# Kernel tuning notes

Hardware: AMD Instinct MI355X
Metric: run time of the kernel (lower is better)

## Reference

```python
import jax, jax.numpy as jnp
import numpy as np

FEAT_DIM = 4
TOKEN_DIM = 256
HIDDEN = [256, 256]
B, N, T = 512, 512, 4
BN_EPS = 1e-5


def setup_inputs() -> dict:
    key = jax.random.key(0)
    ks = jax.random.split(key, 10)
    bbox_ltwh = jax.random.uniform(ks[0], (B, N, T, FEAT_DIM), dtype=jnp.float32)
    mask = jax.random.randint(ks[1], (B, N), 0, 2).astype(bool)
    # MLP params: Linear(4->256)+BN+ReLU, Linear(256->256)+BN+ReLU, Linear(256->256)
    def lin(k, fan_in, fan_out):
        bound = 1.0 / np.sqrt(fan_in)
        kw, kb = jax.random.split(k)
        W = jax.random.uniform(kw, (fan_in, fan_out), minval=-bound, maxval=bound, dtype=jnp.float32)
        b = jax.random.uniform(kb, (fan_out,), minval=-bound, maxval=bound, dtype=jnp.float32)
        return W, b
    W1, b1 = lin(ks[2], FEAT_DIM, HIDDEN[0])
    W2, b2 = lin(ks[3], HIDDEN[0], HIDDEN[1])
    W3, b3 = lin(ks[4], HIDDEN[1], TOKEN_DIM)
    g1 = jnp.ones((HIDDEN[0],), jnp.float32); be1 = jnp.zeros((HIDDEN[0],), jnp.float32)
    g2 = jnp.ones((HIDDEN[1],), jnp.float32); be2 = jnp.zeros((HIDDEN[1],), jnp.float32)
    return {"bbox_ltwh": bbox_ltwh, "mask": mask,
            "W1": W1, "b1": b1, "g1": g1, "be1": be1,
            "W2": W2, "b2": b2, "g2": g2, "be2": be2,
            "W3": W3, "b3": b3}


def _masked_bn(h, m, cnt, gamma, beta):
    # BatchNorm1d (training mode) over only the valid (masked-in) rows.
    mu = jnp.sum(h * m, axis=0) / cnt
    var = jnp.sum(jnp.square(h - mu) * m, axis=0) / cnt
    return (h - mu) * jax.lax.rsqrt(var + BN_EPS) * gamma + beta


def reference(bbox_ltwh, mask, W1, b1, g1, be1, W2, b2, g2, be2, W3, b3):
    # last bbox of each tracklet: [B, N, 4] -> [B*N, 4]
    x = bbox_ltwh[:, :, 0].reshape(-1, FEAT_DIM)
    m = mask.reshape(-1).astype(x.dtype)[:, None]  # [B*N, 1]
    cnt = jnp.maximum(jnp.sum(m), 1.0)
    # Equivalent to gather(valid) -> MLP -> scatter into zeros: compute on all
    # rows with BN statistics taken over valid rows only, then zero invalid rows.
    h = jax.nn.relu(_masked_bn(x @ W1 + b1, m, cnt, g1, be1))
    h = jax.nn.relu(_masked_bn(h @ W2 + b2, m, cnt, g2, be2))
    h = h @ W3 + b3
    out = (h * m).reshape(B, N, TOKEN_DIM)
    return out
```

## Files before the change

### kernel.cpp

```cpp
#include <hip/hip_runtime.h>

typedef __attribute__((ext_vector_type(8))) short short8;
typedef __attribute__((ext_vector_type(4))) float f32x4;

#define M_ROWS (512*512)
#define NTILES (M_ROWS/64)
#define GRID_STATS 512
#define GRID_MLP 256
#define TILES_PER_BLK (NTILES/GRID_MLP)
#define BN_EPS_F 1e-5f

#define WS_FLAG 0
#define WS_P1   64
#define WS_CNT  8192
#define WS_A1   8256
#define WS_D1   9280
#define WS_A2   9536
#define WS_C2   9792
#define WS_W2T  10240
#define WS_W3T  43008
#define WS_P2   76800

__device__ __forceinline__ float load_mask(const void* mp, int fmt, int row) {
  return fmt ? (((const unsigned char*)mp)[row] ? 1.f : 0.f)
             : (((const int*)mp)[row] ? 1.f : 0.f);
}

__device__ __forceinline__ ushort f2bf(float f) {
  unsigned int u = __float_as_uint(f);
  u += 0x7FFFu + ((u >> 16) & 1u);
  return (ushort)(u >> 16);
}

__device__ __forceinline__ void barrier_lds() {
  __builtin_amdgcn_sched_barrier(0);
  asm volatile("s_waitcnt lgkmcnt(0)");
  __builtin_amdgcn_sched_barrier(0);
  __builtin_amdgcn_s_barrier();
  __builtin_amdgcn_sched_barrier(0);
}

__global__ void detect_mask_kernel(const unsigned char* __restrict__ mb,
                                   int* __restrict__ flag) {
  __shared__ int any;
  if (threadIdx.x == 0) any = 0;
  __syncthreads();
  int c = 0;
  for (int i = threadIdx.x; i < 4096; i += blockDim.x)
    if ((i & 3) && mb[i]) c = 1;
  if (c) atomicOr(&any, 1);
  __syncthreads();
  if (threadIdx.x == 0) *flag = any;
}

__global__ __launch_bounds__(256) void stats1_kernel(
    const float* __restrict__ bbox, const void* __restrict__ maskp,
    const int* __restrict__ flagp, float* __restrict__ part) {
  const int t = threadIdx.x;
  const int fmt = *flagp;
  float cnt = 0.f, sx[4] = {0.f,0.f,0.f,0.f}, sxx[16];
  #pragma unroll
  for (int i = 0; i < 16; ++i) sxx[i] = 0.f;
  for (int row = blockIdx.x * 256 + t; row < M_ROWS; row += gridDim.x * 256) {
    float m = load_mask(maskp, fmt, row);
    if (m != 0.f) {
      float4 x = *(const float4*)(bbox + (size_t)row * 16);
      float xv[4] = {x.x, x.y, x.z, x.w};
      cnt += 1.f;
      #pragma unroll
      for (int i = 0; i < 4; ++i) {
        sx[i] += xv[i];
        #pragma unroll
        for (int j = 0; j < 4; ++j) sxx[i*4+j] = fmaf(xv[i], xv[j], sxx[i*4+j]);
      }
    }
  }
  __shared__ float rb[256][22];
  rb[t][0] = cnt;
  #pragma unroll
  for (int i = 0; i < 4; ++i) rb[t][1+i] = sx[i];
  #pragma unroll
  for (int i = 0; i < 16; ++i) rb[t][5+i] = sxx[i];
  __syncthreads();
  for (int off = 128; off > 0; off >>= 1) {
    if (t < off) {
      #pragma unroll
      for (int s = 0; s < 21; ++s) rb[t][s] += rb[t+off][s];
    }
    __syncthreads();
  }
  if (t < 21) part[blockIdx.x * 24 + t] = rb[0][t];
}

__global__ __launch_bounds__(256) void finalize1_kernel(
    const float* __restrict__ part, const float* __restrict__ W1,
    const float* __restrict__ b1, const float* __restrict__ g1,
    const float* __restrict__ be1, float* __restrict__ wsf) {
  const int t = threadIdx.x;
  __shared__ float s[21];
  if (t < 21) {
    float a = 0.f;
    for (int b = 0; b < 256; ++b) a += part[b*24 + t];
    s[t] = a;
  }
  __syncthreads();
  const float cnt = fmaxf(s[0], 1.f);
  float w[4] = {W1[t], W1[256+t], W1[512+t], W1[768+t]};
  const float b1f = b1[t];
  float sw = 0.f;
  #pragma unroll
  for (int k = 0; k < 4; ++k) sw = fmaf(s[1+k], w[k], sw);
  float qf = 0.f;
  #pragma unroll
  for (int i = 0; i < 4; ++i)
    #pragma unroll
    for (int j = 0; j < 4; ++j) qf = fmaf(s[5+i*4+j]*w[i], w[j], qf);
  const float mu  = sw/cnt + b1f;
  const float eh2 = (qf + 2.f*b1f*sw)/cnt + b1f*b1f;
  const float var = fmaxf(eh2 - mu*mu, 0.f);
  const float a1  = g1[t] * rsqrtf(var + BN_EPS_F);
  const float c1  = be1[t] - mu*a1;
  #pragma unroll
  for (int k = 0; k < 4; ++k) wsf[WS_A1 + k*256 + t] = w[k]*a1;
  wsf[WS_D1 + t] = fmaf(b1f, a1, c1);
  if (t == 0) wsf[WS_CNT] = cnt;
}

__global__ __launch_bounds__(256) void prep_weights(
    const float* __restrict__ W2, const float* __restrict__ W3,
    float* __restrict__ wsf) {
  const int n = blockIdx.x & 255;
  const int t = threadIdx.x;
  const float* W = (blockIdx.x < 256) ? W2 : W3;
  ushort* dst = (ushort*)(wsf + ((blockIdx.x < 256) ? WS_W2T : WS_W3T));
  dst[n*256 + t] = f2bf(W[t*256 + n]);
}

__device__ __forceinline__ void compute_h1(
    const float (*xs)[4], ushort* h1s, int t,
    const float a1c[4][2], const float d1c[2]) {
  const int c0 = (t & 127) * 2;
  const int r0 = (t >> 7) * 32;
  #pragma unroll 4
  for (int rr = 0; rr < 32; ++rr) {
    const int r = r0 + rr;
    const f32x4 xv = *(const f32x4*)&xs[r][0];
    float v0 = d1c[0], v1 = d1c[1];
    v0 = fmaf(xv.x, a1c[0][0], v0); v1 = fmaf(xv.x, a1c[0][1], v1);
    v0 = fmaf(xv.y, a1c[1][0], v0); v1 = fmaf(xv.y, a1c[1][1], v1);
    v0 = fmaf(xv.z, a1c[2][0], v0); v1 = fmaf(xv.z, a1c[2][1], v1);
    v0 = fmaf(xv.w, a1c[3][0], v0); v1 = fmaf(xv.w, a1c[3][1], v1);
    v0 = fmaxf(v0, 0.f); v1 = fmaxf(v1, 0.f);
    unsigned int pk = (unsigned int)f2bf(v0) | ((unsigned int)f2bf(v1) << 16);
    unsigned int byte = (unsigned int)r*512u + (unsigned int)c0*2u;
    byte ^= (unsigned int)(r & 7) << 4;
    *(unsigned int*)((char*)h1s + byte) = pk;
  }
}

__device__ __forceinline__ void load_aF(const ushort* h1s, int lane, int ks,
                                        int kb, short8 aF[4]) {
  #pragma unroll
  for (int rf = 0; rf < 4; ++rf) {
    const int row = rf*16 + (lane & 15);
    unsigned int byte = (unsigned int)row*512u + (unsigned int)((ks*32 + kb)*2);
    byte ^= (unsigned int)(row & 7) << 4;
    aF[rf] = *(const short8*)((const char*)h1s + byte);
  }
}

__device__ __forceinline__ void gemm_reg(const ushort* h1s,
    const short8 Br[4][8], int lane, f32x4 acc[4][4]) {
  const int kb = (lane >> 4) * 8;
  #pragma unroll
  for (int ks = 0; ks < 8; ++ks) {
    short8 aF[4];
    load_aF(h1s, lane, ks, kb, aF);
    #pragma unroll
    for (int cf = 0; cf < 4; ++cf)
      #pragma unroll
      for (int rf = 0; rf < 4; ++rf)
        acc[rf][cf] = __builtin_amdgcn_mfma_f32_16x16x32_bf16(
            aF[rf], Br[cf][ks], acc[rf][cf], 0, 0, 0);
  }
}

__device__ __forceinline__ void load_B(const ushort* __restrict__ Wt,
                                       int lane, int wave, short8 Br[4][8]) {
  const int kb = (lane >> 4) * 8;
  const ushort* wp = Wt + (size_t)(wave*64 + (lane & 15))*256 + kb;
  #pragma unroll
  for (int cf = 0; cf < 4; ++cf)
    #pragma unroll
    for (int ks = 0; ks < 8; ++ks)
      Br[cf][ks] = *(const short8*)(wp + cf*4096 + ks*32);
}

__global__ __launch_bounds__(256, 2) void stats2_mfma(
    const float* __restrict__ bbox, const void* __restrict__ maskp,
    const int* __restrict__ flagp, const float* wsf,
    const float* __restrict__ b2, float* __restrict__ part2) {
  __shared__ float xs[64][4];
  __shared__ float ms[64];
  __shared__ ushort h1s[64*256];
  const int t = threadIdx.x, lane = t & 63, wave = t >> 6;
  const int fmt = *flagp;
  float a1c[4][2], d1c[2];
  {
    const int c0 = (t & 127) * 2;
    #pragma unroll
    for (int j = 0; j < 4; ++j) {
      a1c[j][0] = wsf[WS_A1 + j*256 + c0];
      a1c[j][1] = wsf[WS_A1 + j*256 + c0 + 1];
    }
    d1c[0] = wsf[WS_D1 + c0]; d1c[1] = wsf[WS_D1 + c0 + 1];
  }
  short8 B2r[4][8];
  load_B((const ushort*)(wsf + WS_W2T), lane, wave, B2r);
  float b2v[4];
  #pragma unroll
  for (int cf = 0; cf < 4; ++cf) b2v[cf] = b2[wave*64 + cf*16 + (lane & 15)];
  float pS[4] = {0,0,0,0}, pQ[4] = {0,0,0,0};

  for (int tile = blockIdx.x; tile < NTILES; tile += GRID_STATS) {
    const int row0 = tile << 6;
    __syncthreads();
    if (t < 64) {
      float4 x4 = *(const float4*)(bbox + (size_t)(row0 + t) * 16);
      xs[t][0] = x4.x; xs[t][1] = x4.y; xs[t][2] = x4.z; xs[t][3] = x4.w;
      ms[t] = load_mask(maskp, fmt, row0 + t);
    }
    __syncthreads();
    compute_h1(xs, h1s, t, a1c, d1c);
    __syncthreads();
    f32x4 acc[4][4];
    #pragma unroll
    for (int rf = 0; rf < 4; ++rf)
      #pragma unroll
      for (int cf = 0; cf < 4; ++cf)
        acc[rf][cf] = (f32x4){b2v[cf], b2v[cf], b2v[cf], b2v[cf]};
    gemm_reg(h1s, B2r, lane, acc);
    float mr[4][4];
    #pragma unroll
    for (int rf = 0; rf < 4; ++rf)
      #pragma unroll
      for (int r = 0; r < 4; ++r)
        mr[rf][r] = ms[rf*16 + ((lane >> 4) * 4) + r];
    #pragma unroll
    for (int cf = 0; cf < 4; ++cf)
      #pragma unroll
      for (int rf = 0; rf < 4; ++rf)
        #pragma unroll
        for (int r = 0; r < 4; ++r) {
          const float m = mr[rf][r];
          const float v = acc[rf][cf][r];
          pS[cf] = fmaf(m, v, pS[cf]);
          pQ[cf] = fmaf(m*v, v, pQ[cf]);
        }
  }
  #pragma unroll
  for (int cf = 0; cf < 4; ++cf) {
    pS[cf] += __shfl_xor(pS[cf], 16); pS[cf] += __shfl_xor(pS[cf], 32);
    pQ[cf] += __shfl_xor(pQ[cf], 16); pQ[cf] += __shfl_xor(pQ[cf], 32);
  }
  if (lane < 16) {
    #pragma unroll
    for (int cf = 0; cf < 4; ++cf) {
      const int col = wave*64 + cf*16 + lane;
      part2[(size_t)blockIdx.x*512 + col] = pS[cf];
      part2[(size_t)blockIdx.x*512 + 256 + col] = pQ[cf];
    }
  }
}

__global__ __launch_bounds__(256) void finalize2_kernel(
    float* __restrict__ wsf, const float* __restrict__ g2,
    const float* __restrict__ be2) {
  const int f = blockIdx.x, t = threadIdx.x;
  const float* part2 = wsf + WS_P2;
  float s1 = 0.f, s2 = 0.f;
  for (int b = t; b < GRID_STATS; b += 256) {
    s1 += part2[(size_t)b*512 + f];
    s2 += part2[(size_t)b*512 + 256 + f];
  }
  __shared__ float r1[256], r2[256];
  r1[t] = s1; r2[t] = s2;
  __syncthreads();
  for (int off = 128; off > 0; off >>= 1) {
    if (t < off) { r1[t] += r1[t+off]; r2[t] += r2[t+off]; }
    __syncthreads();
  }
  if (t == 0) {
    const float cnt = wsf[WS_CNT];
    const float mu  = r1[0]/cnt;
    const float var = fmaxf(r2[0]/cnt - mu*mu, 0.f);
    const float a2  = g2[f] * rsqrtf(var + BN_EPS_F);
    wsf[WS_A2 + f] = a2;
    wsf[WS_C2 + f] = be2[f] - mu*a2;
  }
}

__global__ __launch_bounds__(256, 1) void mlp3_mfma(
    const float* __restrict__ bbox, const void* __restrict__ maskp,
    const int* __restrict__ flagp, const float* wsf,
    const float* __restrict__ b2, const float* __restrict__ b3,
    float* __restrict__ out) {
  __shared__ ushort h1s[64*256];
  __shared__ float xst[TILES_PER_BLK*64][4];
  __shared__ float mst[TILES_PER_BLK*64];
  const int t = threadIdx.x, lane = t & 63, wave = t >> 6;
  const int fmt = *flagp;
  const int row_base = blockIdx.x * (TILES_PER_BLK*64);

  #pragma unroll
  for (int i = 0; i < TILES_PER_BLK*64/256; ++i) {
    const int r = i*256 + t;
    float4 x4 = *(const float4*)(bbox + (size_t)(row_base + r) * 16);
    xst[r][0] = x4.x; xst[r][1] = x4.y; xst[r][2] = x4.z; xst[r][3] = x4.w;
    mst[r] = load_mask(maskp, fmt, row_base + r);
  }
  float a1c[4][2], d1c[2];
  {
    const int c0 = (t & 127) * 2;
    #pragma unroll
    for (int j = 0; j < 4; ++j) {
      a1c[j][0] = wsf[WS_A1 + j*256 + c0];
      a1c[j][1] = wsf[WS_A1 + j*256 + c0 + 1];
    }
    d1c[0] = wsf[WS_D1 + c0]; d1c[1] = wsf[WS_D1 + c0 + 1];
  }
  short8 B2r[4][8], B3r[4][8];
  load_B((const ushort*)(wsf + WS_W2T), lane, wave, B2r);
  load_B((const ushort*)(wsf + WS_W3T), lane, wave, B3r);
  float b2v[4], b3v[4], a2v[4], c2v[4];
  #pragma unroll
  for (int cf = 0; cf < 4; ++cf) {
    const int col = wave*64 + cf*16 + (lane & 15);
    b2v[cf] = b2[col]; b3v[cf] = b3[col];
    a2v[cf] = wsf[WS_A2 + col]; c2v[cf] = wsf[WS_C2 + col];
  }
  __syncthreads();

  for (int tile = 0; tile < TILES_PER_BLK; ++tile) {
    const int r0 = tile * 64;
    compute_h1(&xst[r0], h1s, t, a1c, d1c);
    barrier_lds();
    f32x4 acc[4][4];
    #pragma unroll
    for (int rf = 0; rf < 4; ++rf)
      #pragma unroll
      for (int cf = 0; cf < 4; ++cf)
        acc[rf][cf] = (f32x4){b2v[cf], b2v[cf], b2v[cf], b2v[cf]};
    gemm_reg(h1s, B2r, lane, acc);
    barrier_lds();
    #pragma unroll
    for (int rf = 0; rf < 4; ++rf)
      #pragma unroll
      for (int cf = 0; cf < 4; ++cf) {
        const int col = wave*64 + cf*16 + (lane & 15);
        #pragma unroll
        for (int r = 0; r < 4; ++r) {
          const float v = fmaxf(fmaf(acc[rf][cf][r], a2v[cf], c2v[cf]), 0.f);
          const int row = rf*16 + ((lane >> 4) * 4) + r;
          unsigned int byte = (unsigned int)row*512u + (unsigned int)col*2u;
          byte ^= (unsigned int)(row & 7) << 4;
          *(ushort*)((char*)h1s + byte) = f2bf(v);
        }
      }
    barrier_lds();
    #pragma unroll
    for (int rf = 0; rf < 4; ++rf)
      #pragma unroll
      for (int cf = 0; cf < 4; ++cf)
        acc[rf][cf] = (f32x4){b3v[cf], b3v[cf], b3v[cf], b3v[cf]};
    gemm_reg(h1s, B3r, lane, acc);
    float mr[4][4];
    #pragma unroll
    for (int rf = 0; rf < 4; ++rf)
      #pragma unroll
      for (int r = 0; r < 4; ++r)
        mr[rf][r] = mst[r0 + rf*16 + ((lane >> 4) * 4) + r];
    #pragma unroll
    for (int rf = 0; rf < 4; ++rf)
      #pragma unroll
      for (int cf = 0; cf < 4; ++cf) {
        const int col = wave*64 + cf*16 + (lane & 15);
        #pragma unroll
        for (int r = 0; r < 4; ++r) {
          const int lrow = rf*16 + ((lane >> 4) * 4) + r;
          out[(size_t)(row_base + r0 + lrow)*256 + col] =
              acc[rf][cf][r] * mr[rf][r];
        }
      }
    barrier_lds();
  }
}

extern "C" void kernel_launch(void* const* d_in, const int* in_sizes, int n_in,
                              void* d_out, int out_size, void* d_ws, size_t ws_size,
                              hipStream_t stream) {
  (void)in_sizes; (void)n_in; (void)out_size; (void)ws_size;
  const float* bbox = (const float*)d_in[0];
  const void*  maskp= d_in[1];
  const float* W1 = (const float*)d_in[2];
  const float* b1 = (const float*)d_in[3];
  const float* g1 = (const float*)d_in[4];
  const float* be1= (const float*)d_in[5];
  const float* W2 = (const float*)d_in[6];
  const float* b2 = (const float*)d_in[7];
  const float* g2 = (const float*)d_in[8];
  const float* be2= (const float*)d_in[9];
  const float* W3 = (const float*)d_in[10];
  const float* b3 = (const float*)d_in[11];
  float* out = (float*)d_out;
  float* wsf = (float*)d_ws;
  int*   flag= (int*)d_ws;

  hipLaunchKernelGGL(detect_mask_kernel, dim3(1), dim3(256), 0, stream,
                     (const unsigned char*)maskp, flag);
  hipLaunchKernelGGL(stats1_kernel, dim3(256), dim3(256), 0, stream,
                     bbox, maskp, flag, wsf + WS_P1);
  hipLaunchKernelGGL(finalize1_kernel, dim3(1), dim3(256), 0, stream,
                     wsf + WS_P1, W1, b1, g1, be1, wsf);
  hipLaunchKernelGGL(prep_weights, dim3(512), dim3(256), 0, stream,
                     W2, W3, wsf);
  hipLaunchKernelGGL(stats2_mfma, dim3(GRID_STATS), dim3(256), 0, stream,
                     bbox, maskp, flag, wsf, b2, wsf + WS_P2);
  hipLaunchKernelGGL(finalize2_kernel, dim3(256), dim3(256), 0, stream,
                     wsf, g2, be2);
  hipLaunchKernelGGL(mlp3_mfma, dim3(GRID_MLP), dim3(256), 0, stream,
                     bbox, maskp, flag, wsf, b2, b3, out);
}
```

Baseline: 217.1 us.

## Fuse all MLP stages into one cooperative kernel with grid syncs

Replaces the seven-kernel pipeline with a single cooperative kernel of 256 blocks. It computes layer-1 stats, weight transpose, layer-2 stats and the final MLP, separated by grid-wide syncs. Each block keeps its 1024 input rows and masks resident in LDS across phases, so bbox is read once instead of three times. Launch overhead is also reduced. In exchange it runs only 256 blocks with one block per CU, adds three grid barriers, and the weight transpose now writes in a strided pattern. The old multi-kernel path remains as a fallback if the cooperative launch fails.

```diff
diff --git a/kernel.cpp b/kernel.cpp
--- a/kernel.cpp
+++ b/kernel.cpp
@@ -1,16 +1,21 @@
 #include <hip/hip_runtime.h>
+#include <hip/hip_cooperative_groups.h>
+
+namespace cg = cooperative_groups;
 
 typedef __attribute__((ext_vector_type(8))) short short8;
 typedef __attribute__((ext_vector_type(4))) float f32x4;
 
 #define M_ROWS (512*512)
 #define NTILES (M_ROWS/64)
+#define GRID_N 256
+#define ROWS_PER_BLK (M_ROWS/GRID_N)
+#define TILES_PER_BLK (ROWS_PER_BLK/64)
 #define GRID_STATS 512
 #define GRID_MLP 256
-#define TILES_PER_BLK (NTILES/GRID_MLP)
+#define TPB_FALL (NTILES/GRID_MLP)
 #define BN_EPS_F 1e-5f
 
-#define WS_FLAG 0
 #define WS_P1   64
 #define WS_CNT  8192
 #define WS_A1   8256
@@ -38,102 +43,6 @@
   __builtin_amdgcn_sched_barrier(0);
   __builtin_amdgcn_s_barrier();
   __builtin_amdgcn_sched_barrier(0);
-}
-
-__global__ void detect_mask_kernel(const unsigned char* __restrict__ mb,
-                                   int* __restrict__ flag) {
-  __shared__ int any;
-  if (threadIdx.x == 0) any = 0;
-  __syncthreads();
-  int c = 0;
-  for (int i = threadIdx.x; i < 4096; i += blockDim.x)
-    if ((i & 3) && mb[i]) c = 1;
-  if (c) atomicOr(&any, 1);
-  __syncthreads();
-  if (threadIdx.x == 0) *flag = any;
-}
-
-__global__ __launch_bounds__(256) void stats1_kernel(
-    const float* __restrict__ bbox, const void* __restrict__ maskp,
-    const int* __restrict__ flagp, float* __restrict__ part) {
-  const int t = threadIdx.x;
-  const int fmt = *flagp;
-  float cnt = 0.f, sx[4] = {0.f,0.f,0.f,0.f}, sxx[16];
-  #pragma unroll
-  for (int i = 0; i < 16; ++i) sxx[i] = 0.f;
-  for (int row = blockIdx.x * 256 + t; row < M_ROWS; row += gridDim.x * 256) {
-    float m = load_mask(maskp, fmt, row);
-    if (m != 0.f) {
-      float4 x = *(const float4*)(bbox + (size_t)row * 16);
-      float xv[4] = {x.x, x.y, x.z, x.w};
-      cnt += 1.f;
-      #pragma unroll
-      for (int i = 0; i < 4; ++i) {
-        sx[i] += xv[i];
-        #pragma unroll
-        for (int j = 0; j < 4; ++j) sxx[i*4+j] = fmaf(xv[i], xv[j], sxx[i*4+j]);
-      }
-    }
-  }
-  __shared__ float rb[256][22];
-  rb[t][0] = cnt;
-  #pragma unroll
-  for (int i = 0; i < 4; ++i) rb[t][1+i] = sx[i];
-  #pragma unroll
-  for (int i = 0; i < 16; ++i) rb[t][5+i] = sxx[i];
-  __syncthreads();
-  for (int off = 128; off > 0; off >>= 1) {
-    if (t < off) {
-      #pragma unroll
-      for (int s = 0; s < 21; ++s) rb[t][s] += rb[t+off][s];
-    }
-    __syncthreads();
-  }
-  if (t < 21) part[blockIdx.x * 24 + t] = rb[0][t];
-}
-
-__global__ __launch_bounds__(256) void finalize1_kernel(
-    const float* __restrict__ part, const float* __restrict__ W1,
-    const float* __restrict__ b1, const float* __restrict__ g1,
-    const float* __restrict__ be1, float* __restrict__ wsf) {
-  const int t = threadIdx.x;
-  __shared__ float s[21];
-  if (t < 21) {
-    float a = 0.f;
-    for (int b = 0; b < 256; ++b) a += part[b*24 + t];
-    s[t] = a;
-  }
-  __syncthreads();
-  const float cnt = fmaxf(s[0], 1.f);
-  float w[4] = {W1[t], W1[256+t], W1[512+t], W1[768+t]};
-  const float b1f = b1[t];
-  float sw = 0.f;
-  #pragma unroll
-  for (int k = 0; k < 4; ++k) sw = fmaf(s[1+k], w[k], sw);
-  float qf = 0.f;
-  #pragma unroll
-  for (int i = 0; i < 4; ++i)
-    #pragma unroll
-    for (int j = 0; j < 4; ++j) qf = fmaf(s[5+i*4+j]*w[i], w[j], qf);
-  const float mu  = sw/cnt + b1f;
-  const float eh2 = (qf + 2.f*b1f*sw)/cnt + b1f*b1f;
-  const float var = fmaxf(eh2 - mu*mu, 0.f);
-  const float a1  = g1[t] * rsqrtf(var + BN_EPS_F);
-  const float c1  = be1[t] - mu*a1;
-  #pragma unroll
-  for (int k = 0; k < 4; ++k) wsf[WS_A1 + k*256 + t] = w[k]*a1;
-  wsf[WS_D1 + t] = fmaf(b1f, a1, c1);
-  if (t == 0) wsf[WS_CNT] = cnt;
-}
-
-__global__ __launch_bounds__(256) void prep_weights(
-    const float* __restrict__ W2, const float* __restrict__ W3,
-    float* __restrict__ wsf) {
-  const int n = blockIdx.x & 255;
-  const int t = threadIdx.x;
-  const float* W = (blockIdx.x < 256) ? W2 : W3;
-  ushort* dst = (ushort*)(wsf + ((blockIdx.x < 256) ? WS_W2T : WS_W3T));
-  dst[n*256 + t] = f2bf(W[t*256 + n]);
 }
 
 __device__ __forceinline__ void compute_h1(
@@ -196,6 +105,362 @@
       Br[cf][ks] = *(const short8*)(wp + cf*4096 + ks*32);
 }
 
+__global__ void __launch_bounds__(256, 1) fused_all(
+    const float* __restrict__ bbox, const void* __restrict__ maskp,
+    const float* __restrict__ W1, const float* __restrict__ b1,
+    const float* __restrict__ g1, const float* __restrict__ be1,
+    const float* __restrict__ W2, const float* __restrict__ b2,
+    const float* __restrict__ g2, const float* __restrict__ be2,
+    const float* __restrict__ W3, const float* __restrict__ b3,
+    float* __restrict__ out, float* __restrict__ wsf) {
+  cg::grid_group grid = cg::this_grid();
+  __shared__ float xst[ROWS_PER_BLK][4];
+  __shared__ float mst[ROWS_PER_BLK];
+  __shared__ ushort h1s[64*256];
+  __shared__ int s_fmt;
+  float (*red)[24] = (float (*)[24])(void*)h1s;
+  const int t = threadIdx.x, lane = t & 63, wave = t >> 6;
+  const int b = blockIdx.x;
+  const int row_base = b * ROWS_PER_BLK;
+
+  if (t == 0) s_fmt = 0;
+  __syncthreads();
+  {
+    const uint4 v = ((const uint4*)maskp)[t];
+    if (((v.x | v.y | v.z | v.w) & 0xFFFFFF00u) != 0u) s_fmt = 1;
+  }
+  __syncthreads();
+  const int fmt = s_fmt;
+
+  {
+    float cnt = 0.f, sx[4] = {0.f,0.f,0.f,0.f}, sxx[16];
+    #pragma unroll
+    for (int i = 0; i < 16; ++i) sxx[i] = 0.f;
+    #pragma unroll
+    for (int i = 0; i < ROWS_PER_BLK/256; ++i) {
+      const int r = i*256 + t;
+      float4 x4 = *(const float4*)(bbox + (size_t)(row_base + r) * 16);
+      xst[r][0] = x4.x; xst[r][1] = x4.y; xst[r][2] = x4.z; xst[r][3] = x4.w;
+      const float m = load_mask(maskp, fmt, row_base + r);
+      mst[r] = m;
+      if (m != 0.f) {
+        float xv[4] = {x4.x, x4.y, x4.z, x4.w};
+        cnt += 1.f;
+        #pragma unroll
+        for (int i2 = 0; i2 < 4; ++i2) {
+          sx[i2] += xv[i2];
+          #pragma unroll
+          for (int j = 0; j < 4; ++j)
+            sxx[i2*4+j] = fmaf(xv[i2], xv[j], sxx[i2*4+j]);
+        }
+      }
+    }
+    red[t][0] = cnt;
+    #pragma unroll
+    for (int i = 0; i < 4; ++i) red[t][1+i] = sx[i];
+    #pragma unroll
+    for (int i = 0; i < 16; ++i) red[t][5+i] = sxx[i];
+    __syncthreads();
+    for (int off = 128; off > 0; off >>= 1) {
+      if (t < off) {
+        #pragma unroll
+        for (int s = 0; s < 21; ++s) red[t][s] += red[t+off][s];
+      }
+      __syncthreads();
+    }
+    if (t < 21) wsf[WS_P1 + b*24 + t] = red[0][t];
+  }
+  {
+    ((ushort*)(wsf + WS_W2T))[t*256 + b] = f2bf(W2[b*256 + t]);
+    ((ushort*)(wsf + WS_W3T))[t*256 + b] = f2bf(W3[b*256 + t]);
+  }
+  grid.sync();
+
+  float a1c[4][2], d1c[2], cnt_all;
+  {
+    #pragma unroll
+    for (int s = 0; s < 21; ++s) red[t][s] = wsf[WS_P1 + t*24 + s];
+    __syncthreads();
+    for (int off = 128; off > 0; off >>= 1) {
+      if (t < off) {
+        #pragma unroll
+        for (int s = 0; s < 21; ++s) red[t][s] += red[t+off][s];
+      }
+      __syncthreads();
+    }
+    float s[21];
+    #pragma unroll
+    for (int i = 0; i < 21; ++i) s[i] = red[0][i];
+    __syncthreads();
+    cnt_all = fmaxf(s[0], 1.f);
+    const int c0 = (t & 127) * 2;
+    #pragma unroll
+    for (int cc = 0; cc < 2; ++cc) {
+      const int f = c0 + cc;
+      float w[4] = {W1[f], W1[256+f], W1[512+f], W1[768+f]};
+      const float b1f = b1[f];
+      float sw = 0.f;
+      #pragma unroll
+      for (int k = 0; k < 4; ++k) sw = fmaf(s[1+k], w[k], sw);
+      float qf = 0.f;
+      #pragma unroll
+      for (int i = 0; i < 4; ++i)
+        #pragma unroll
+        for (int j = 0; j < 4; ++j) qf = fmaf(s[5+i*4+j]*w[i], w[j], qf);
+      const float mu  = sw/cnt_all + b1f;
+      const float eh2 = (qf + 2.f*b1f*sw)/cnt_all + b1f*b1f;
+      const float var = fmaxf(eh2 - mu*mu, 0.f);
+      const float a1  = g1[f] * rsqrtf(var + BN_EPS_F);
+      const float c1  = be1[f] - mu*a1;
+      #pragma unroll
+      for (int k = 0; k < 4; ++k) a1c[k][cc] = w[k]*a1;
+      d1c[cc] = fmaf(b1f, a1, c1);
+    }
+  }
+
+  short8 B2r[4][8];
+  load_B((const ushort*)(wsf + WS_W2T), lane, wave, B2r);
+  float b2v[4];
+  #pragma unroll
+  for (int cf = 0; cf < 4; ++cf) b2v[cf] = b2[wave*64 + cf*16 + (lane & 15)];
+  {
+    float pS[4] = {0,0,0,0}, pQ[4] = {0,0,0,0};
+    for (int tile = 0; tile < TILES_PER_BLK; ++tile) {
+      compute_h1(&xst[tile*64], h1s, t, a1c, d1c);
+      __syncthreads();
+      f32x4 acc[4][4];
+      #pragma unroll
+      for (int rf = 0; rf < 4; ++rf)
+        #pragma unroll
+        for (int cf = 0; cf < 4; ++cf)
+          acc[rf][cf] = (f32x4){b2v[cf], b2v[cf], b2v[cf], b2v[cf]};
+      gemm_reg(h1s, B2r, lane, acc);
+      #pragma unroll
+      for (int rf = 0; rf < 4; ++rf) {
+        #pragma unroll
+        for (int r = 0; r < 4; ++r) {
+          const float m = mst[tile*64 + rf*16 + ((lane >> 4) * 4) + r];
+          #pragma unroll
+          for (int cf = 0; cf < 4; ++cf) {
+            const float v = acc[rf][cf][r];
+            pS[cf] = fmaf(m, v, pS[cf]);
+            pQ[cf] = fmaf(m*v, v, pQ[cf]);
+          }
+        }
+      }
+      __syncthreads();
+    }
+    #pragma unroll
+    for (int cf = 0; cf < 4; ++cf) {
+      pS[cf] += __shfl_xor(pS[cf], 16); pS[cf] += __shfl_xor(pS[cf], 32);
+      pQ[cf] += __shfl_xor(pQ[cf], 16); pQ[cf] += __shfl_xor(pQ[cf], 32);
+    }
+    if (lane < 16) {
+      #pragma unroll
+      for (int cf = 0; cf < 4; ++cf) {
+        const int col = wave*64 + cf*16 + lane;
+        wsf[WS_P2 + (size_t)col*256 + b] = pS[cf];
+        wsf[WS_P2 + (size_t)(256 + col)*256 + b] = pQ[cf];
+      }
+    }
+  }
+  grid.sync();
+
+  {
+    float s1 = wsf[WS_P2 + (size_t)b*256 + t];
+    float s2 = wsf[WS_P2 + (size_t)(256 + b)*256 + t];
+    red[t][0] = s1; red[t][1] = s2;
+    __syncthreads();
+    for (int off = 128; off > 0; off >>= 1) {
+      if (t < off) { red[t][0] += red[t+off][0]; red[t][1] += red[t+off][1]; }
+      __syncthreads();
+    }
+    if (t == 0) {
+      const float mu  = red[0][0]/cnt_all;
+      const float var = fmaxf(red[0][1]/cnt_all - mu*mu, 0.f);
+      const float a2  = g2[b] * rsqrtf(var + BN_EPS_F);
+      wsf[WS_A2 + b] = a2;
+      wsf[WS_C2 + b] = be2[b] - mu*a2;
+    }
+  }
+  grid.sync();
+
+  short8 B3r[4][8];
+  load_B((const ushort*)(wsf + WS_W3T), lane, wave, B3r);
+  float b3v[4], a2v[4], c2v[4];
+  #pragma unroll
+  for (int cf = 0; cf < 4; ++cf) {
+    const int col = wave*64 + cf*16 + (lane & 15);
+    b3v[cf] = b3[col];
+    a2v[cf] = wsf[WS_A2 + col]; c2v[cf] = wsf[WS_C2 + col];
+  }
+  __syncthreads();
+
+  for (int tile = 0; tile < TILES_PER_BLK; ++tile) {
+    const int r0 = tile * 64;
+    compute_h1(&xst[r0], h1s, t, a1c, d1c);
+    barrier_lds();
+    f32x4 acc[4][4];
+    #pragma unroll
+    for (int rf = 0; rf < 4; ++rf)
+      #pragma unroll
+      for (int cf = 0; cf < 4; ++cf)
+        acc[rf][cf] = (f32x4){b2v[cf], b2v[cf], b2v[cf], b2v[cf]};
+    gemm_reg(h1s, B2r, lane, acc);
+    barrier_lds();
+    #pragma unroll
+    for (int rf = 0; rf < 4; ++rf)
+      #pragma unroll
+      for (int cf = 0; cf < 4; ++cf) {
+        const int col = wave*64 + cf*16 + (lane & 15);
+        #pragma unroll
+        for (int r = 0; r < 4; ++r) {
+          const float v = fmaxf(fmaf(acc[rf][cf][r], a2v[cf], c2v[cf]), 0.f);
+          const int row = rf*16 + ((lane >> 4) * 4) + r;
+          unsigned int byte = (unsigned int)row*512u + (unsigned int)col*2u;
+          byte ^= (unsigned int)(row & 7) << 4;
+          *(ushort*)((char*)h1s + byte) = f2bf(v);
+        }
+      }
+    barrier_lds();
+    #pragma unroll
+    for (int rf = 0; rf < 4; ++rf)
+      #pragma unroll
+      for (int cf = 0; cf < 4; ++cf)
+        acc[rf][cf] = (f32x4){b3v[cf], b3v[cf], b3v[cf], b3v[cf]};
+    gemm_reg(h1s, B3r, lane, acc);
+    float mr[4][4];
+    #pragma unroll
+    for (int rf = 0; rf < 4; ++rf)
+      #pragma unroll
+      for (int r = 0; r < 4; ++r)
+        mr[rf][r] = mst[r0 + rf*16 + ((lane >> 4) * 4) + r];
+    #pragma unroll
+    for (int rf = 0; rf < 4; ++rf)
+      #pragma unroll
+      for (int cf = 0; cf < 4; ++cf) {
+        const int col = wave*64 + cf*16 + (lane & 15);
+        #pragma unroll
+        for (int r = 0; r < 4; ++r) {
+          const int lrow = rf*16 + ((lane >> 4) * 4) + r;
+          out[(size_t)(row_base + r0 + lrow)*256 + col] =
+              acc[rf][cf][r] * mr[rf][r];
+        }
+      }
+    barrier_lds();
+  }
+}
+
+__global__ void detect_mask_kernel(const unsigned char* __restrict__ mb,
+                                   int* __restrict__ flag) {
+  __shared__ int any;
+  if (threadIdx.x == 0) any = 0;
+  __syncthreads();
+  int c = 0;
+  for (int i = threadIdx.x; i < 4096; i += blockDim.x)
+    if ((i & 3) && mb[i]) c = 1;
+  if (c) atomicOr(&any, 1);
+  __syncthreads();
+  if (threadIdx.x == 0) *flag = any;
+}
+
+__global__ __launch_bounds__(256) void stats1_kernel(
+    const float* __restrict__ bbox, const void* __restrict__ maskp,
+    const int* __restrict__ flagp, float* __restrict__ part) {
+  const int t = threadIdx.x;
+  const int fmt = *flagp;
+  float cnt = 0.f, sx[4] = {0.f,0.f,0.f,0.f}, sxx[16];
+  #pragma unroll
+  for (int i = 0; i < 16; ++i) sxx[i] = 0.f;
+  for (int row = blockIdx.x * 256 + t; row < M_ROWS; row += gridDim.x * 256) {
+    float m = load_mask(maskp, fmt, row);
+    if (m != 0.f) {
+      float4 x = *(const float4*)(bbox + (size_t)row * 16);
+      float xv[4] = {x.x, x.y, x.z, x.w};
+      cnt += 1.f;
+      #pragma unroll
+      for (int i = 0; i < 4; ++i) {
+        sx[i] += xv[i];
+        #pragma unroll
+        for (int j = 0; j < 4; ++j) sxx[i*4+j] = fmaf(xv[i], xv[j], sxx[i*4+j]);
+      }
+    }
+  }
+  __shared__ float rb[256][22];
+  rb[t][0] = cnt;
+  #pragma unroll
+  for (int i = 0; i < 4; ++i) rb[t][1+i] = sx[i];
+  #pragma unroll
+  for (int i = 0; i < 16; ++i) rb[t][5+i] = sxx[i];
+  __syncthreads();
+  for (int off = 128; off > 0; off >>= 1) {
+    if (t < off) {
+      #pragma unroll
+      for (int s = 0; s < 21; ++s) rb[t][s] += rb[t+off][s];
+    }
+    __syncthreads();
+  }
+  if (t < 21) part[blockIdx.x * 24 + t] = rb[0][t];
+}
+
+__global__ __launch_bounds__(256) void finalize1_kernel(
+    const float* __restrict__ part, const float* __restrict__ W1,
+    const float* __restrict__ b1, const float* __restrict__ g1,
+    const float* __restrict__ be1, float* __restrict__ wsf) {
+  const int t = threadIdx.x;
+  __shared__ float s[21];
+  if (t < 21) {
+    float a = 0.f;
+    for (int b = 0; b < 256; ++b) a += part[b*24 + t];
+    s[t] = a;
+  }
+  __syncthreads();
+  const float cnt = fmaxf(s[0], 1.f);
+  float w[4] = {W1[t], W1[256+t], W1[512+t], W1[768+t]};
+  const float b1f = b1[t];
+  float sw = 0.f;
+  #pragma unroll
+  for (int k = 0; k < 4; ++k) sw = fmaf(s[1+k], w[k], sw);
+  float qf = 0.f;
+  #pragma unroll
+  for (int i = 0; i < 4; ++i)
+    #pragma unroll
+    for (int j = 0; j < 4; ++j) qf = fmaf(s[5+i*4+j]*w[i], w[j], qf);
+  const float mu  = sw/cnt + b1f;
+  const float eh2 = (qf + 2.f*b1f*sw)/cnt + b1f*b1f;
+  const float var = fmaxf(eh2 - mu*mu, 0.f);
+  const float a1  = g1[t] * rsqrtf(var + BN_EPS_F);
+  const float c1  = be1[t] - mu*a1;
+  #pragma unroll
+  for (int k = 0; k < 4; ++k) wsf[WS_A1 + k*256 + t] = w[k]*a1;
+  wsf[WS_D1 + t] = fmaf(b1f, a1, c1);
+  if (t == 0) wsf[WS_CNT] = cnt;
+}
+
+__global__ __launch_bounds__(256) void prep_weights(
+    const float* __restrict__ W2, const float* __restrict__ W3,
+    float* __restrict__ wsf) {
+  const int n = blockIdx.x & 255;
+  const int t = threadIdx.x;
+  const float* W = (blockIdx.x < 256) ? W2 : W3;
+  ushort* dst = (ushort*)(wsf + ((blockIdx.x < 256) ? WS_W2T : WS_W3T));
+  dst[n*256 + t] = f2bf(W[t*256 + n]);
+}
+
+__device__ __forceinline__ void fb_compute_h1(
+    const float (*xs)[4], ushort* h1s, int t,
+    const float* wsf) {
+  float a1c[4][2], d1c[2];
+  const int c0 = (t & 127) * 2;
+  #pragma unroll
+  for (int j = 0; j < 4; ++j) {
+    a1c[j][0] = wsf[WS_A1 + j*256 + c0];
+    a1c[j][1] = wsf[WS_A1 + j*256 + c0 + 1];
+  }
+  d1c[0] = wsf[WS_D1 + c0]; d1c[1] = wsf[WS_D1 + c0 + 1];
+  compute_h1(xs, h1s, t, a1c, d1c);
+}
+
 __global__ __launch_bounds__(256, 2) void stats2_mfma(
     const float* __restrict__ bbox, const void* __restrict__ maskp,
     const int* __restrict__ flagp, const float* wsf,
@@ -306,14 +571,14 @@
     const float* __restrict__ b2, const float* __restrict__ b3,
     float* __restrict__ out) {
   __shared__ ushort h1s[64*256];
-  __shared__ float xst[TILES_PER_BLK*64][4];
-  __shared__ float mst[TILES_PER_BLK*64];
+  __shared__ float xst[TPB_FALL*64][4];
+  __shared__ float mst[TPB_FALL*64];
   const int t = threadIdx.x, lane = t & 63, wave = t >> 6;
   const int fmt = *flagp;
-  const int row_base = blockIdx.x * (TILES_PER_BLK*64);
-
-  #pragma unroll
-  for (int i = 0; i < TILES_PER_BLK*64/256; ++i) {
+  const int row_base = blockIdx.x * (TPB_FALL*64);
+
+  #pragma unroll
+  for (int i = 0; i < TPB_FALL*64/256; ++i) {
     const int r = i*256 + t;
     float4 x4 = *(const float4*)(bbox + (size_t)(row_base + r) * 16);
     xst[r][0] = x4.x; xst[r][1] = x4.y; xst[r][2] = x4.z; xst[r][3] = x4.w;
@@ -341,7 +606,7 @@
   }
   __syncthreads();
 
-  for (int tile = 0; tile < TILES_PER_BLK; ++tile) {
+  for (int tile = 0; tile < TPB_FALL; ++tile) {
     const int r0 = tile * 64;
     compute_h1(&xst[r0], h1s, t, a1c, d1c);
     barrier_lds();
@@ -416,18 +681,28 @@
   float* wsf = (float*)d_ws;
   int*   flag= (int*)d_ws;
 
-  hipLaunchKernelGGL(detect_mask_kernel, dim3(1), dim3(256), 0, stream,
-                     (const unsigned char*)maskp, flag);
-  hipLaunchKernelGGL(stats1_kernel, dim3(256), dim3(256), 0, stream,
-                     bbox, maskp, flag, wsf + WS_P1);
-  hipLaunchKernelGGL(finalize1_kernel, dim3(1), dim3(256), 0, stream,
-                     wsf + WS_P1, W1, b1, g1, be1, wsf);
-  hipLaunchKernelGGL(prep_weights, dim3(512), dim3(256), 0, stream,
-                     W2, W3, wsf);
-  hipLaunchKernelGGL(stats2_mfma, dim3(GRID_STATS), dim3(256), 0, stream,
-                     bbox, maskp, flag, wsf, b2, wsf + WS_P2);
-  hipLaunchKernelGGL(finalize2_kernel, dim3(256), dim3(256), 0, stream,
-                     wsf, g2, be2);
-  hipLaunchKernelGGL(mlp3_mfma, dim3(GRID_MLP), dim3(256), 0, stream,
-                     bbox, maskp, flag, wsf, b2, b3, out);
-}
+  void* args[] = {
+    (void*)&bbox, (void*)&maskp, (void*)&W1, (void*)&b1, (void*)&g1,
+    (void*)&be1, (void*)&W2, (void*)&b2, (void*)&g2, (void*)&be2,
+    (void*)&W3, (void*)&b3, (void*)&out, (void*)&wsf
+  };
+  hipError_t err = hipLaunchCooperativeKernel((const void*)fused_all,
+                                              dim3(GRID_N), dim3(256),
+                                              args, 0, stream);
+  if (err != hipSuccess) {
+    hipLaunchKernelGGL(detect_mask_kernel, dim3(1), dim3(256), 0, stream,
+                       (const unsigned char*)maskp, flag);
+    hipLaunchKernelGGL(stats1_kernel, dim3(256), dim3(256), 0, stream,
+                       bbox, maskp, flag, wsf + WS_P1);
+    hipLaunchKernelGGL(finalize1_kernel, dim3(1), dim3(256), 0, stream,
+                       wsf + WS_P1, W1, b1, g1, be1, wsf);
+    hipLaunchKernelGGL(prep_weights, dim3(512), dim3(256), 0, stream,
+                       W2, W3, wsf);
+    hipLaunchKernelGGL(stats2_mfma, dim3(GRID_STATS), dim3(256), 0, stream,
+                       bbox, maskp, flag, wsf, b2, wsf + WS_P2);
+    hipLaunchKernelGGL(finalize2_kernel, dim3(256), dim3(256), 0, stream,
+                       wsf, g2, be2);
+    hipLaunchKernelGGL(mlp3_mfma, dim3(GRID_MLP), dim3(256), 0, stream,
+                       bbox, maskp, flag, wsf, b2, b3, out);
+  }
+}
```

Measured after the change: 304.2 us. 1.4x slower.

## Merge setup kernels and widen final MLP kernel to 512 threads

Applied to the files above, without the earlier changes.

Folds mask-format detection, first-layer statistics and weight transpose/bf16 conversion into a single setup kernel, removing two launches, and makes each consumer kernel detect the mask format locally instead of reading a flag. The final MLP kernel now uses 512 threads (8 waves), each owning 32 output columns instead of 64. This halves per-wave B registers and accumulators and allows two blocks per CU, aiming for better latency hiding. The cost is a two-stage reduction in finalize1 and extra per-block mask detection work.

```diff
diff --git a/kernel.cpp b/kernel.cpp
--- a/kernel.cpp
+++ b/kernel.cpp
@@ -5,21 +5,22 @@
 
 #define M_ROWS (512*512)
 #define NTILES (M_ROWS/64)
+#define GRID_SETUP 512
 #define GRID_STATS 512
 #define GRID_MLP 256
-#define TILES_PER_BLK (NTILES/GRID_MLP)
+#define ROWS_MLP (M_ROWS/GRID_MLP)
+#define TILES_MLP (ROWS_MLP/64)
 #define BN_EPS_F 1e-5f
 
-#define WS_FLAG 0
 #define WS_P1   64
-#define WS_CNT  8192
-#define WS_A1   8256
-#define WS_D1   9280
-#define WS_A2   9536
-#define WS_C2   9792
-#define WS_W2T  10240
-#define WS_W3T  43008
-#define WS_P2   76800
+#define WS_CNT  12352
+#define WS_A1   12416
+#define WS_D1   13440
+#define WS_A2   13696
+#define WS_C2   13952
+#define WS_W2T  14336
+#define WS_W3T  47104
+#define WS_P2   79872
 
 __device__ __forceinline__ float load_mask(const void* mp, int fmt, int row) {
   return fmt ? (((const unsigned char*)mp)[row] ? 1.f : 0.f)
@@ -38,102 +39,6 @@
   __builtin_amdgcn_sched_barrier(0);
   __builtin_amdgcn_s_barrier();
   __builtin_amdgcn_sched_barrier(0);
-}
-
-__global__ void detect_mask_kernel(const unsigned char* __restrict__ mb,
-                                   int* __restrict__ flag) {
-  __shared__ int any;
-  if (threadIdx.x == 0) any = 0;
-  __syncthreads();
-  int c = 0;
-  for (int i = threadIdx.x; i < 4096; i += blockDim.x)
-    if ((i & 3) && mb[i]) c = 1;
-  if (c) atomicOr(&any, 1);
-  __syncthreads();
-  if (threadIdx.x == 0) *flag = any;
-}
-
-__global__ __launch_bounds__(256) void stats1_kernel(
-    const float* __restrict__ bbox, const void* __restrict__ maskp,
-    const int* __restrict__ flagp, float* __restrict__ part) {
-  const int t = threadIdx.x;
-  const int fmt = *flagp;
-  float cnt = 0.f, sx[4] = {0.f,0.f,0.f,0.f}, sxx[16];
-  #pragma unroll
-  for (int i = 0; i < 16; ++i) sxx[i] = 0.f;
-  for (int row = blockIdx.x * 256 + t; row < M_ROWS; row += gridDim.x * 256) {
-    float m = load_mask(maskp, fmt, row);
-    if (m != 0.f) {
-      float4 x = *(const float4*)(bbox + (size_t)row * 16);
-      float xv[4] = {x.x, x.y, x.z, x.w};
-      cnt += 1.f;
-      #pragma unroll
-      for (int i = 0; i < 4; ++i) {
-        sx[i] += xv[i];
-        #pragma unroll
-        for (int j = 0; j < 4; ++j) sxx[i*4+j] = fmaf(xv[i], xv[j], sxx[i*4+j]);
-      }
-    }
-  }
-  __shared__ float rb[256][22];
-  rb[t][0] = cnt;
-  #pragma unroll
-  for (int i = 0; i < 4; ++i) rb[t][1+i] = sx[i];
-  #pragma unroll
-  for (int i = 0; i < 16; ++i) rb[t][5+i] = sxx[i];
-  __syncthreads();
-  for (int off = 128; off > 0; off >>= 1) {
-    if (t < off) {
-      #pragma unroll
-      for (int s = 0; s < 21; ++s) rb[t][s] += rb[t+off][s];
-    }
-    __syncthreads();
-  }
-  if (t < 21) part[blockIdx.x * 24 + t] = rb[0][t];
-}
-
-__global__ __launch_bounds__(256) void finalize1_kernel(
-    const float* __restrict__ part, const float* __restrict__ W1,
-    const float* __restrict__ b1, const float* __restrict__ g1,
-    const float* __restrict__ be1, float* __restrict__ wsf) {
-  const int t = threadIdx.x;
-  __shared__ float s[21];
-  if (t < 21) {
-    float a = 0.f;
-    for (int b = 0; b < 256; ++b) a += part[b*24 + t];
-    s[t] = a;
-  }
-  __syncthreads();
-  const float cnt = fmaxf(s[0], 1.f);
-  float w[4] = {W1[t], W1[256+t], W1[512+t], W1[768+t]};
-  const float b1f = b1[t];
-  float sw = 0.f;
-  #pragma unroll
-  for (int k = 0; k < 4; ++k) sw = fmaf(s[1+k], w[k], sw);
-  float qf = 0.f;
-  #pragma unroll
-  for (int i = 0; i < 4; ++i)
-    #pragma unroll
-    for (int j = 0; j < 4; ++j) qf = fmaf(s[5+i*4+j]*w[i], w[j], qf);
-  const float mu  = sw/cnt + b1f;
-  const float eh2 = (qf + 2.f*b1f*sw)/cnt + b1f*b1f;
-  const float var = fmaxf(eh2 - mu*mu, 0.f);
-  const float a1  = g1[t] * rsqrtf(var + BN_EPS_F);
-  const float c1  = be1[t] - mu*a1;
-  #pragma unroll
-  for (int k = 0; k < 4; ++k) wsf[WS_A1 + k*256 + t] = w[k]*a1;
-  wsf[WS_D1 + t] = fmaf(b1f, a1, c1);
-  if (t == 0) wsf[WS_CNT] = cnt;
-}
-
-__global__ __launch_bounds__(256) void prep_weights(
-    const float* __restrict__ W2, const float* __restrict__ W3,
-    float* __restrict__ wsf) {
-  const int n = blockIdx.x & 255;
-  const int t = threadIdx.x;
-  const float* W = (blockIdx.x < 256) ? W2 : W3;
-  ushort* dst = (ushort*)(wsf + ((blockIdx.x < 256) ? WS_W2T : WS_W3T));
-  dst[n*256 + t] = f2bf(W[t*256 + n]);
 }
 
 __device__ __forceinline__ void compute_h1(
@@ -158,6 +63,28 @@
   }
 }
 
+__device__ __forceinline__ void compute_h1_512(
+    const float (*xs)[4], ushort* h1s, int t,
+    const float a1c[4][2], const float d1c[2]) {
+  const int c0 = (t & 127) * 2;
+  const int r0 = (t >> 7) * 16;
+  #pragma unroll 4
+  for (int rr = 0; rr < 16; ++rr) {
+    const int r = r0 + rr;
+    const f32x4 xv = *(const f32x4*)&xs[r][0];
+    float v0 = d1c[0], v1 = d1c[1];
+    v0 = fmaf(xv.x, a1c[0][0], v0); v1 = fmaf(xv.x, a1c[0][1], v1);
+    v0 = fmaf(xv.y, a1c[1][0], v0); v1 = fmaf(xv.y, a1c[1][1], v1);
+    v0 = fmaf(xv.z, a1c[2][0], v0); v1 = fmaf(xv.z, a1c[2][1], v1);
+    v0 = fmaf(xv.w, a1c[3][0], v0); v1 = fmaf(xv.w, a1c[3][1], v1);
+    v0 = fmaxf(v0, 0.f); v1 = fmaxf(v1, 0.f);
+    unsigned int pk = (unsigned int)f2bf(v0) | ((unsigned int)f2bf(v1) << 16);
+    unsigned int byte = (unsigned int)r*512u + (unsigned int)c0*2u;
+    byte ^= (unsigned int)(r & 7) << 4;
+    *(unsigned int*)((char*)h1s + byte) = pk;
+  }
+}
+
 __device__ __forceinline__ void load_aF(const ushort* h1s, int lane, int ks,
                                         int kb, short8 aF[4]) {
   #pragma unroll
@@ -196,15 +123,151 @@
       Br[cf][ks] = *(const short8*)(wp + cf*4096 + ks*32);
 }
 
+__device__ __forceinline__ void gemm_reg2(const ushort* h1s,
+    const short8 Br[2][8], int lane, f32x4 acc[4][2]) {
+  const int kb = (lane >> 4) * 8;
+  #pragma unroll
+  for (int ks = 0; ks < 8; ++ks) {
+    short8 aF[4];
+    load_aF(h1s, lane, ks, kb, aF);
+    #pragma unroll
+    for (int cf = 0; cf < 2; ++cf)
+      #pragma unroll
+      for (int rf = 0; rf < 4; ++rf)
+        acc[rf][cf] = __builtin_amdgcn_mfma_f32_16x16x32_bf16(
+            aF[rf], Br[cf][ks], acc[rf][cf], 0, 0, 0);
+  }
+}
+
+__device__ __forceinline__ void load_B2(const ushort* __restrict__ Wt,
+                                        int lane, int wave, short8 Br[2][8]) {
+  const int kb = (lane >> 4) * 8;
+  const ushort* wp = Wt + (size_t)(wave*32 + (lane & 15))*256 + kb;
+  #pragma unroll
+  for (int cf = 0; cf < 2; ++cf)
+    #pragma unroll
+    for (int ks = 0; ks < 8; ++ks)
+      Br[cf][ks] = *(const short8*)(wp + cf*4096 + ks*32);
+}
+
+__global__ __launch_bounds__(256) void setup_kernel(
+    const float* __restrict__ bbox, const void* __restrict__ maskp,
+    const float* __restrict__ W2, const float* __restrict__ W3,
+    float* __restrict__ wsf) {
+  __shared__ int s_fmt;
+  __shared__ float red[256][22];
+  const int t = threadIdx.x, b = blockIdx.x;
+  if (t == 0) s_fmt = 0;
+  __syncthreads();
+  {
+    const uint4 v = ((const uint4*)maskp)[t];
+    if (((v.x | v.y | v.z | v.w) & 0xFFFFFF00u) != 0u) s_fmt = 1;
+  }
+  __syncthreads();
+  const int fmt = s_fmt;
+
+  float own[21];
+  #pragma unroll
+  for (int i = 0; i < 21; ++i) own[i] = 0.f;
+  #pragma unroll
+  for (int i = 0; i < 2; ++i) {
+    const int row = b*512 + i*256 + t;
+    const float m = load_mask(maskp, fmt, row);
+    if (m != 0.f) {
+      float4 x4 = *(const float4*)(bbox + (size_t)row * 16);
+      float xv[4] = {x4.x, x4.y, x4.z, x4.w};
+      own[0] += 1.f;
+      #pragma unroll
+      for (int i2 = 0; i2 < 4; ++i2) {
+        own[1+i2] += xv[i2];
+        #pragma unroll
+        for (int j = 0; j < 4; ++j)
+          own[5+i2*4+j] = fmaf(xv[i2], xv[j], own[5+i2*4+j]);
+      }
+    }
+  }
+  #pragma unroll
+  for (int s = 0; s < 21; ++s) red[t][s] = own[s];
+  __syncthreads();
+  for (int off = 128; off > 0; off >>= 1) {
+    if (t < off) {
+      #pragma unroll
+      for (int s = 0; s < 21; ++s) red[t][s] += red[t+off][s];
+    }
+    __syncthreads();
+  }
+  if (t < 21) wsf[WS_P1 + b*24 + t] = red[0][t];
+
+  if (b < 256) {
+    ((ushort*)(wsf + WS_W2T))[t*256 + b] = f2bf(W2[b*256 + t]);
+  } else {
+    const int bb = b - 256;
+    ((ushort*)(wsf + WS_W3T))[t*256 + bb] = f2bf(W3[bb*256 + t]);
+  }
+}
+
+__global__ __launch_bounds__(256) void finalize1_kernel(
+    const float* __restrict__ part, const float* __restrict__ W1,
+    const float* __restrict__ b1, const float* __restrict__ g1,
+    const float* __restrict__ be1, float* __restrict__ wsf) {
+  __shared__ float red[256][22];
+  __shared__ float sarr[21];
+  const int t = threadIdx.x;
+  #pragma unroll
+  for (int s = 0; s < 21; ++s)
+    red[t][s] = part[t*24 + s] + part[(t+256)*24 + s];
+  __syncthreads();
+  for (int off = 128; off > 0; off >>= 1) {
+    if (t < off) {
+      #pragma unroll
+      for (int s = 0; s < 21; ++s) red[t][s] += red[t+off][s];
+    }
+    __syncthreads();
+  }
+  if (t < 21) sarr[t] = red[0][t];
+  __syncthreads();
+  float s[21];
+  #pragma unroll
+  for (int i = 0; i < 21; ++i) s[i] = sarr[i];
+  const float cnt = fmaxf(s[0], 1.f);
+  float w[4] = {W1[t], W1[256+t], W1[512+t], W1[768+t]};
+  const float b1f = b1[t];
+  float sw = 0.f;
+  #pragma unroll
+  for (int k = 0; k < 4; ++k) sw = fmaf(s[1+k], w[k], sw);
+  float qf = 0.f;
+  #pragma unroll
+  for (int i = 0; i < 4; ++i)
+    #pragma unroll
+    for (int j = 0; j < 4; ++j) qf = fmaf(s[5+i*4+j]*w[i], w[j], qf);
+  const float mu  = sw/cnt + b1f;
+  const float eh2 = (qf + 2.f*b1f*sw)/cnt + b1f*b1f;
+  const float var = fmaxf(eh2 - mu*mu, 0.f);
+  const float a1  = g1[t] * rsqrtf(var + BN_EPS_F);
+  const float c1  = be1[t] - mu*a1;
+  #pragma unroll
+  for (int k = 0; k < 4; ++k) wsf[WS_A1 + k*256 + t] = w[k]*a1;
+  wsf[WS_D1 + t] = fmaf(b1f, a1, c1);
+  if (t == 0) wsf[WS_CNT] = cnt;
+}
+
 __global__ __launch_bounds__(256, 2) void stats2_mfma(
     const float* __restrict__ bbox, const void* __restrict__ maskp,
-    const int* __restrict__ flagp, const float* wsf,
-    const float* __restrict__ b2, float* __restrict__ part2) {
+    const float* wsf, const float* __restrict__ b2,
+    float* __restrict__ part2) {
   __shared__ float xs[64][4];
   __shared__ float ms[64];
   __shared__ ushort h1s[64*256];
+  __shared__ int s_fmt;
   const int t = threadIdx.x, lane = t & 63, wave = t >> 6;
-  const int fmt = *flagp;
+  if (t == 0) s_fmt = 0;
+  __syncthreads();
+  {
+    const uint4 v = ((const uint4*)maskp)[t];
+    if (((v.x | v.y | v.z | v.w) & 0xFFFFFF00u) != 0u) s_fmt = 1;
+  }
+  __syncthreads();
+  const int fmt = s_fmt;
   float a1c[4][2], d1c[2];
   {
     const int c0 = (t & 127) * 2;
@@ -300,21 +363,28 @@
   }
 }
 
-__global__ __launch_bounds__(256, 1) void mlp3_mfma(
+__global__ __launch_bounds__(512, 2) void mlp3_512(
     const float* __restrict__ bbox, const void* __restrict__ maskp,
-    const int* __restrict__ flagp, const float* wsf,
-    const float* __restrict__ b2, const float* __restrict__ b3,
-    float* __restrict__ out) {
+    const float* wsf, const float* __restrict__ b2,
+    const float* __restrict__ b3, float* __restrict__ out) {
+  __shared__ float xst[ROWS_MLP][4];
+  __shared__ float mst[ROWS_MLP];
   __shared__ ushort h1s[64*256];
-  __shared__ float xst[TILES_PER_BLK*64][4];
-  __shared__ float mst[TILES_PER_BLK*64];
+  __shared__ int s_fmt;
   const int t = threadIdx.x, lane = t & 63, wave = t >> 6;
-  const int fmt = *flagp;
-  const int row_base = blockIdx.x * (TILES_PER_BLK*64);
-
-  #pragma unroll
-  for (int i = 0; i < TILES_PER_BLK*64/256; ++i) {
-    const int r = i*256 + t;
+  if (t == 0) s_fmt = 0;
+  __syncthreads();
+  if (t < 256) {
+    const uint4 v = ((const uint4*)maskp)[t];
+    if (((v.x | v.y | v.z | v.w) & 0xFFFFFF00u) != 0u) s_fmt = 1;
+  }
+  __syncthreads();
+  const int fmt = s_fmt;
+  const int row_base = blockIdx.x * ROWS_MLP;
+
+  #pragma unroll
+  for (int i = 0; i < ROWS_MLP/512; ++i) {
+    const int r = i*512 + t;
     float4 x4 = *(const float4*)(bbox + (size_t)(row_base + r) * 16);
     xst[r][0] = x4.x; xst[r][1] = x4.y; xst[r][2] = x4.z; xst[r][3] = x4.w;
     mst[r] = load_mask(maskp, fmt, row_base + r);
@@ -329,35 +399,35 @@
     }
     d1c[0] = wsf[WS_D1 + c0]; d1c[1] = wsf[WS_D1 + c0 + 1];
   }
-  short8 B2r[4][8], B3r[4][8];
-  load_B((const ushort*)(wsf + WS_W2T), lane, wave, B2r);
-  load_B((const ushort*)(wsf + WS_W3T), lane, wave, B3r);
-  float b2v[4], b3v[4], a2v[4], c2v[4];
-  #pragma unroll
-  for (int cf = 0; cf < 4; ++cf) {
-    const int col = wave*64 + cf*16 + (lane & 15);
+  short8 B2r[2][8], B3r[2][8];
+  load_B2((const ushort*)(wsf + WS_W2T), lane, wave, B2r);
+  load_B2((const ushort*)(wsf + WS_W3T), lane, wave, B3r);
+  float b2v[2], b3v[2], a2v[2], c2v[2];
+  #pragma unroll
+  for (int cf = 0; cf < 2; ++cf) {
+    const int col = wave*32 + cf*16 + (lane & 15);
     b2v[cf] = b2[col]; b3v[cf] = b3[col];
     a2v[cf] = wsf[WS_A2 + col]; c2v[cf] = wsf[WS_C2 + col];
   }
   __syncthreads();
 
-  for (int tile = 0; tile < TILES_PER_BLK; ++tile) {
+  for (int tile = 0; tile < TILES_MLP; ++tile) {
     const int r0 = tile * 64;
-    compute_h1(&xst[r0], h1s, t, a1c, d1c);
+    compute_h1_512(&xst[r0], h1s, t, a1c, d1c);
     barrier_lds();
-    f32x4 acc[4][4];
-    #pragma unroll
-    for (int rf = 0; rf < 4; ++rf)
-      #pragma unroll
-      for (int cf = 0; cf < 4; ++cf)
+    f32x4 acc[4][2];
+    #pragma unroll
+    for (int rf = 0; rf < 4; ++rf)
+      #pragma unroll
+      for (int cf = 0; cf < 2; ++cf)
         acc[rf][cf] = (f32x4){b2v[cf], b2v[cf], b2v[cf], b2v[cf]};
-    gemm_reg(h1s, B2r, lane, acc);
+    gemm_reg2(h1s, B2r, lane, acc);
     barrier_lds();
     #pragma unroll
     for (int rf = 0; rf < 4; ++rf)
       #pragma unroll
-      for (int cf = 0; cf < 4; ++cf) {
-        const int col = wave*64 + cf*16 + (lane & 15);
+      for (int cf = 0; cf < 2; ++cf) {
+        const int col = wave*32 + cf*16 + (lane & 15);
         #pragma unroll
         for (int r = 0; r < 4; ++r) {
           const float v = fmaxf(fmaf(acc[rf][cf][r], a2v[cf], c2v[cf]), 0.f);
@@ -371,9 +441,9 @@
     #pragma unroll
     for (int rf = 0; rf < 4; ++rf)
       #pragma unroll
-      for (int cf = 0; cf < 4; ++cf)
+      for (int cf = 0; cf < 2; ++cf)
         acc[rf][cf] = (f32x4){b3v[cf], b3v[cf], b3v[cf], b3v[cf]};
-    gemm_reg(h1s, B3r, lane, acc);
+    gemm_reg2(h1s, B3r, lane, acc);
     float mr[4][4];
     #pragma unroll
     for (int rf = 0; rf < 4; ++rf)
@@ -383,8 +453,8 @@
     #pragma unroll
     for (int rf = 0; rf < 4; ++rf)
       #pragma unroll
-      for (int cf = 0; cf < 4; ++cf) {
-        const int col = wave*64 + cf*16 + (lane & 15);
+      for (int cf = 0; cf < 2; ++cf) {
+        const int col = wave*32 + cf*16 + (lane & 15);
         #pragma unroll
         for (int r = 0; r < 4; ++r) {
           const int lrow = rf*16 + ((lane >> 4) * 4) + r;
@@ -414,20 +484,15 @@
   const float* b3 = (const float*)d_in[11];
   float* out = (float*)d_out;
   float* wsf = (float*)d_ws;
-  int*   flag= (int*)d_ws;
-
-  hipLaunchKernelGGL(detect_mask_kernel, dim3(1), dim3(256), 0, stream,
-                     (const unsigned char*)maskp, flag);
-  hipLaunchKernelGGL(stats1_kernel, dim3(256), dim3(256), 0, stream,
-                     bbox, maskp, flag, wsf + WS_P1);
+
+  hipLaunchKernelGGL(setup_kernel, dim3(GRID_SETUP), dim3(256), 0, stream,
+                     bbox, maskp, W2, W3, wsf);
   hipLaunchKernelGGL(finalize1_kernel, dim3(1), dim3(256), 0, stream,
                      wsf + WS_P1, W1, b1, g1, be1, wsf);
-  hipLaunchKernelGGL(prep_weights, dim3(512), dim3(256), 0, stream,
-                     W2, W3, wsf);
   hipLaunchKernelGGL(stats2_mfma, dim3(GRID_STATS), dim3(256), 0, stream,
-                     bbox, maskp, flag, wsf, b2, wsf + WS_P2);
+                     bbox, maskp, wsf, b2, wsf + WS_P2);
   hipLaunchKernelGGL(finalize2_kernel, dim3(256), dim3(256), 0, stream,
                      wsf, g2, be2);
-  hipLaunchKernelGGL(mlp3_mfma, dim3(GRID_MLP), dim3(256), 0, stream,
-                     bbox, maskp, flag, wsf, b2, b3, out);
-}
+  hipLaunchKernelGGL(mlp3_512, dim3(GRID_MLP), dim3(512), 0, stream,
+                     bbox, maskp, wsf, b2, b3, out);
+}
```

After: 306.8 us. 41.3% more time.
